# Kernel optimization log

Measured on AMD Instinct MI355X. Metric: run time of the kernel, lower is better.

The kernel has to match this reference:

```python
import jax, jax.numpy as jnp
import numpy as np

N_ATOMS = 8_000_000
N_REC = 2_000_000
N_POC = 500_000
N_CHAINS = 4


def setup_inputs() -> dict:
    key = jax.random.key(0)
    k1, k2, k3, k4 = jax.random.split(key, 4)
    # coordinates in nm, inside a ~5 nm box
    positions = jax.random.uniform(k1, (N_ATOMS, 3), dtype=jnp.float32) * 5.0
    box_vectors = jnp.diag(jnp.array([5.0, 5.0, 5.0], dtype=jnp.float32))
    # unique receptor atom indices into positions
    rec_indices = jax.random.permutation(k2, N_ATOMS)[:N_REC].astype(jnp.int32)
    # unique pocket indices INTO THE REC ARRAY (poc_pos = rec_pos[poc_indices])
    poc_indices = jax.random.permutation(k3, N_REC)[:N_POC].astype(jnp.int32)
    # contiguous chain assignment over rec atoms, all chains present in pocket
    chain_ids = ((jnp.arange(N_REC, dtype=jnp.int32) * N_CHAINS) // N_REC).astype(jnp.int32)
    poc_chain_ids = chain_ids[poc_indices]
    ref_poc = jax.random.uniform(k4, (N_POC, 3), dtype=jnp.float32) * 5.0
    k = jnp.float32(100.0)  # kJ/mol/nm^2
    return {
        "positions": positions, "box_vectors": box_vectors, "ref_poc": ref_poc,
        "k": k, "rec_indices": rec_indices, "poc_indices": poc_indices,
        "chain_ids": chain_ids, "poc_chain_ids": poc_chain_ids, "n_chains": N_CHAINS,
    }


def best_periodic_translation(pos1, pos2, box_vectors):
    # pos1, pos2: [C,3]; box_vectors: [3,3] (rows are lattice vectors)
    delta = pos2 - pos1
    inv = 1.0 / jnp.diag(box_vectors)
    s3 = jnp.round(delta[:, 2] * inv[2])
    delta = delta - s3[:, None] * box_vectors[2]
    s2 = jnp.round(delta[:, 1] * inv[1])
    delta = delta - s2[:, None] * box_vectors[1]
    s1 = jnp.round(delta[:, 0] * inv[0])
    return s1[:, None] * box_vectors[0] + s2[:, None] * box_vectors[1] + s3[:, None] * box_vectors[2]


def reference(positions, box_vectors, ref_poc, k, rec_indices, poc_indices, chain_ids, poc_chain_ids, n_chains):
    rec_pos = positions[rec_indices]  # [R,3]
    # Per-chain pocket COM. NOTE: original indexes global positions here
    # (positions[poc_chain_indices]), NOT rec_pos -- reproduced faithfully.
    poc_glob = positions[poc_indices]  # [P,3]
    counts = jax.ops.segment_sum(jnp.ones((poc_glob.shape[0],), poc_glob.dtype), poc_chain_ids, num_segments=n_chains)  # [C]
    poc_com = jax.ops.segment_sum(poc_glob, poc_chain_ids, num_segments=n_chains) / counts[:, None]  # [C,3]
    ref_com = jax.ops.segment_sum(ref_poc, poc_chain_ids, num_segments=n_chains) / counts[:, None]  # [C,3]
    best_t = best_periodic_translation(poc_com, ref_com, box_vectors)  # [C,3]
    rec_pos = rec_pos + best_t[chain_ids]  # translate each chain into the reference image

    poc_pos = rec_pos[poc_indices]  # [P,3]
    rec_origin = jnp.mean(rec_pos, axis=0)
    rec_centered = rec_pos - rec_origin
    r_sq = jnp.sum(rec_centered ** 2, axis=1)  # [R]
    F = jnp.zeros_like(rec_pos).at[poc_indices].set(-2.0 * k * (poc_pos - ref_poc))
    F_mean = jnp.mean(F, axis=0)
    torque = jnp.cross(rec_centered, F)
    torque_mean = jnp.mean(torque, axis=0)
    F_rot = jnp.cross(torque_mean[None], rec_centered) / r_sq[:, None]
    F_final = jnp.zeros_like(positions).at[rec_indices].set(F_mean + F_rot)
    return (jnp.float32(0.0), F_final)
```

## Files before the change

### kernel.cpp

```cpp
#include <hip/hip_runtime.h>


typedef unsigned int uint32;
typedef unsigned char uchar;

#define MAXC 16
#define W_BT 0
#define W_O 48
#define W_FM 52
#define W_TM 56
#define W_ACC 64

#define GCOUNT_OFF 4096
#define REC_OFF 8192
#define NB 512
#define BSH 14
#define BUCKET_ATOMS (1 << BSH)
#define CAP 5120
#define INV8_OFF (REC_OFF + NB * CAP * 4)

#define PB 512
#define RB 512
#define K1_KPT 16
#define K1_CHUNK (256 * K1_KPT)

struct PartSh { uint32 hist[NB]; uint32 curs[NB]; uint32 base[NB]; };
struct PocSh  { float red[4][43]; float accL[3 + MAXC * 10]; };
union ShU { PartSh part; PocSh poc; };

__device__ inline float waveSum(float v) {
#pragma unroll
  for (int off = 32; off > 0; off >>= 1) v += __shfl_down(v, off, 64);
  return v;
}

__global__ __launch_bounds__(256) void k_fused(
    const float* __restrict__ pos, const float* __restrict__ ref_poc,
    const int* __restrict__ rec_idx, const int* __restrict__ cid,
    const int* __restrict__ poc_idx, const int* __restrict__ poc_cid,
    const int* __restrict__ ncp, int R, int P,
    uint32* __restrict__ gcount, uint32* __restrict__ grecords,
    float* __restrict__ ws) {
  const int tid = threadIdx.x;
  const int bid = blockIdx.x;
  __shared__ ShU sh;
  const int C = ncp[0];

  if (bid < PB) {
    const int gsz = PB * 256;
    if (C <= 4) {
      float vals[43];
#pragma unroll
      for (int v = 0; v < 43; ++v) vals[v] = 0.f;
      for (int rb = bid * 256 + tid; rb < P; rb += 4 * gsz) {
        int rr[4], i2[4], c2[4], ri[4];
        float g[4][3], p[4][3], rf[4][3];
#pragma unroll
        for (int q = 0; q < 4; ++q) {
          int r = rb + q * gsz;
          rr[q] = (r < P) ? r : -1;
        }
#pragma unroll
        for (int q = 0; q < 4; ++q) {
          int r = (rr[q] < 0) ? 0 : rr[q];
          i2[q] = poc_idx[r];
          c2[q] = poc_cid[r];
        }
#pragma unroll
        for (int q = 0; q < 4; ++q) {
          ri[q] = rec_idx[i2[q]];
          g[q][0] = pos[3 * i2[q] + 0];
          g[q][1] = pos[3 * i2[q] + 1];
          g[q][2] = pos[3 * i2[q] + 2];
        }
#pragma unroll
        for (int q = 0; q < 4; ++q) {
          int r = (rr[q] < 0) ? 0 : rr[q];
          p[q][0] = pos[3 * ri[q] + 0];
          p[q][1] = pos[3 * ri[q] + 1];
          p[q][2] = pos[3 * ri[q] + 2];
          rf[q][0] = ref_poc[3 * r + 0];
          rf[q][1] = ref_poc[3 * r + 1];
          rf[q][2] = ref_poc[3 * r + 2];
        }
#pragma unroll
        for (int q = 0; q < 4; ++q) {
          if (rr[q] >= 0) {
            vals[0] += p[q][1] * rf[q][2] - p[q][2] * rf[q][1];
            vals[1] += p[q][2] * rf[q][0] - p[q][0] * rf[q][2];
            vals[2] += p[q][0] * rf[q][1] - p[q][1] * rf[q][0];
#pragma unroll
            for (int cc = 0; cc < 4; ++cc) {
              bool m = (c2[q] == cc);
              float* a = &vals[3 + cc * 10];
              a[0] += m ? g[q][0] : 0.f; a[1] += m ? g[q][1] : 0.f;
              a[2] += m ? g[q][2] : 0.f;
              a[3] += m ? rf[q][0] : 0.f; a[4] += m ? rf[q][1] : 0.f;
              a[5] += m ? rf[q][2] : 0.f;
              a[6] += m ? p[q][0] : 0.f; a[7] += m ? p[q][1] : 0.f;
              a[8] += m ? p[q][2] : 0.f;
              a[9] += m ? 1.f : 0.f;
            }
          }
        }
      }
      const int wid = tid >> 6;
#pragma unroll
      for (int v = 0; v < 43; ++v) {
        float s = waveSum(vals[v]);
        if ((tid & 63) == 0) sh.poc.red[wid][v] = s;
      }
      __syncthreads();
      for (int t = tid; t < 43; t += 256)
        atomicAdd(&ws[W_ACC + 19 + t], sh.poc.red[0][t] + sh.poc.red[1][t] +
                                       sh.poc.red[2][t] + sh.poc.red[3][t]);
    } else {
      float* accL = sh.poc.accL;
      for (int t = tid; t < 3 + MAXC * 10; t += 256) accL[t] = 0.f;
      __syncthreads();
      for (int r = bid * 256 + tid; r < P; r += PB * 256) {
        int i2 = poc_idx[r];
        int c2 = poc_cid[r];
        int ri = rec_idx[i2];
        float gx = pos[3 * i2 + 0], gy = pos[3 * i2 + 1], gz = pos[3 * i2 + 2];
        float px = pos[3 * ri + 0], py = pos[3 * ri + 1], pz = pos[3 * ri + 2];
        float rx = ref_poc[3 * r + 0], ry = ref_poc[3 * r + 1], rz = ref_poc[3 * r + 2];
        atomicAdd(&accL[0], py * rz - pz * ry);
        atomicAdd(&accL[1], pz * rx - px * rz);
        atomicAdd(&accL[2], px * ry - py * rx);
        float* a = &accL[3 + c2 * 10];
        atomicAdd(&a[0], gx); atomicAdd(&a[1], gy); atomicAdd(&a[2], gz);
        atomicAdd(&a[3], rx); atomicAdd(&a[4], ry); atomicAdd(&a[5], rz);
        atomicAdd(&a[6], px); atomicAdd(&a[7], py); atomicAdd(&a[8], pz);
        atomicAdd(&a[9], 1.f);
      }
      __syncthreads();
      for (int t = tid; t < 3 + MAXC * 10; t += 256)
        if (accL[t] != 0.f) atomicAdd(&ws[W_ACC + 19 + t], accL[t]);
    }
  } else {
    const int pb = bid - PB;
    uint32* hist = sh.part.hist;
    uint32* curs = sh.part.curs;
    uint32* base = sh.part.base;
    for (int r0 = pb * K1_CHUNK; r0 < R; r0 += RB * K1_CHUNK) {
      int cnt = R - r0; if (cnt > K1_CHUNK) cnt = K1_CHUNK;
      for (int t = tid; t < NB; t += 256) { hist[t] = 0u; curs[t] = 0u; }
      __syncthreads();
      uint32 enc[K1_KPT];
#pragma unroll
      for (int j = 0; j < K1_KPT; ++j) {
        int t = tid + j * 256;
        uint32 e = 0xFFFFFFFFu;
        if (t < cnt) {
          uint32 idx = (uint32)rec_idx[r0 + t];
          uint32 c = (uint32)cid[r0 + t] & 255u;
          e = (idx << 8) | c;
          atomicAdd(&hist[idx >> BSH], 1u);
        }
        enc[j] = e;
      }
      __syncthreads();
      for (int t = tid; t < NB; t += 256) {
        uint32 h = hist[t];
        base[t] = h ? atomicAdd(&gcount[t], h) : 0u;
      }
      __syncthreads();
#pragma unroll
      for (int j = 0; j < K1_KPT; ++j) {
        uint32 e = enc[j];
        if (e != 0xFFFFFFFFu) {
          uint32 b = e >> (8 + BSH);
          uint32 slot = base[b] + atomicAdd(&curs[b], 1u);
          if (slot < CAP) grecords[b * CAP + slot] = e;
        }
      }
      __syncthreads();
    }
  }
}

__global__ __launch_bounds__(256) void k_bucket_build(
    const float4* __restrict__ pos4, const int* __restrict__ ncp,
    const uint32* __restrict__ gcount, const uint32* __restrict__ grecords,
    int N, uchar* __restrict__ inv8, float* __restrict__ ws) {
  const int tid = threadIdx.x;
  const int b = blockIdx.x;
  const int a0 = b << BSH;
  if (a0 >= N) return;
  int natoms = N - a0; if (natoms > BUCKET_ATOMS) natoms = BUCKET_ATOMS;

  __shared__ uchar map_[BUCKET_ATOMS];
  __shared__ float cnt16[MAXC];
  uint4* m16 = (uint4*)map_;
  uint4 ff; ff.x = ff.y = ff.z = ff.w = 0xFFFFFFFFu;
  for (int t = tid; t < BUCKET_ATOMS / 16; t += 256) m16[t] = ff;
  const int C = ncp[0];
  if (C > 4) for (int t = tid; t < MAXC; t += 256) cnt16[t] = 0.f;
  __syncthreads();

  int n = (int)gcount[b]; if (n > CAP) n = CAP;
  float c0 = 0.f, c1 = 0.f, c2 = 0.f, c3 = 0.f;
  for (int t = tid; t < n; t += 256) {
    uint32 e = grecords[b * CAP + t];
    uint32 ia = (e >> 8) & (BUCKET_ATOMS - 1);
    uint32 c = e & 255u;
    map_[ia] = (uchar)c;
    if (C <= 4) {
      c0 += (c == 0u) ? 1.f : 0.f;
      c1 += (c == 1u) ? 1.f : 0.f;
      c2 += (c == 2u) ? 1.f : 0.f;
      c3 += (c == 3u) ? 1.f : 0.f;
    } else {
      atomicAdd(&cnt16[c], 1.f);
    }
  }
  __syncthreads();

  uchar* dst = inv8 + a0;
  if (natoms == BUCKET_ATOMS) {
    uint4* d16 = (uint4*)dst;
    for (int t = tid; t < BUCKET_ATOMS / 16; t += 256) d16[t] = m16[t];
  } else {
    for (int t = tid; t < natoms; t += 256) dst[t] = map_[t];
  }

  float sx = 0.f, sy = 0.f, sz = 0.f;
  int ngf = natoms >> 2;
  const uchar4* m4 = (const uchar4*)map_;
  int g0 = a0 >> 2;
  for (int g = tid; g < ngf; g += 256) {
    float4 p0 = pos4[3 * (g0 + g) + 0];
    float4 p1 = pos4[3 * (g0 + g) + 1];
    float4 p2 = pos4[3 * (g0 + g) + 2];
    uchar4 m = m4[g];
    if (m.x != 255) { sx += p0.x; sy += p0.y; sz += p0.z; }
    if (m.y != 255) { sx += p0.w; sy += p1.x; sz += p1.y; }
    if (m.z != 255) { sx += p1.z; sy += p1.w; sz += p2.x; }
    if (m.w != 255) { sx += p2.y; sy += p2.z; sz += p2.w; }
  }
  int tb = natoms & 3;
  if (tid < tb) {
    int a = a0 + (ngf << 2) + tid;
    const float* pf = (const float*)pos4;
    if (map_[(ngf << 2) + tid] != 255) {
      sx += pf[3 * a]; sy += pf[3 * a + 1]; sz += pf[3 * a + 2];
    }
  }

  __shared__ float red[4][7];
  float vv[7] = {sx, sy, sz, c0, c1, c2, c3};
  const int wid = tid >> 6;
#pragma unroll
  for (int v = 0; v < 7; ++v) {
    float s = waveSum(vv[v]);
    if ((tid & 63) == 0) red[wid][v] = s;
  }
  __syncthreads();
  if (tid < 7) {
    float s = red[0][tid] + red[1][tid] + red[2][tid] + red[3][tid];
    atomicAdd(&ws[W_ACC + tid], s);
  }
  if (C > 4 && tid < C) atomicAdd(&ws[W_ACC + 3 + tid], cnt16[tid]);
}

__global__ void k_finalize(const float* __restrict__ box,
                           const float* __restrict__ kp,
                           const int* __restrict__ ncp,
                           int R, float* __restrict__ ws) {
  __shared__ float tot[192];
  const int C = ncp[0];
  for (int t = threadIdx.x; t < 192; t += blockDim.x) tot[t] = ws[W_ACC + t];
  __syncthreads();
  if (threadIdx.x != 0) return;
  const float kk = kp[0];
  const float Rf = (float)R;
  const float* xp = &tot[19];
  float inv0 = 1.f / box[0], inv1 = 1.f / box[4], inv2 = 1.f / box[8];
  float ox = tot[0], oy = tot[1], oz = tot[2];
  float Fx = 0, Fy = 0, Fz = 0;
  float T1x = 0, T1y = 0, T1z = 0, T2x = 0, T2y = 0, T2z = 0;
  for (int c = 0; c < C; ++c) {
    float nrec = tot[3 + c];
    const float* a = &tot[22 + c * 10];
    float np = a[9];
    float invn = 1.f / np;
    float pcx = a[0] * invn, pcy = a[1] * invn, pcz = a[2] * invn;
    float rcx = a[3] * invn, rcy = a[4] * invn, rcz = a[5] * invn;
    float dx = rcx - pcx, dy = rcy - pcy, dz = rcz - pcz;
    float s3 = rintf(dz * inv2);
    dx -= s3 * box[6]; dy -= s3 * box[7]; dz -= s3 * box[8];
    float s2 = rintf(dy * inv1);
    dx -= s2 * box[3]; dy -= s2 * box[4]; dz -= s2 * box[5];
    float s1 = rintf(dx * inv0);
    float btx = s1 * box[0] + s2 * box[3] + s3 * box[6];
    float bty = s1 * box[1] + s2 * box[4] + s3 * box[7];
    float btz = s1 * box[2] + s2 * box[5] + s3 * box[8];
    ws[W_BT + c * 3 + 0] = btx;
    ws[W_BT + c * 3 + 1] = bty;
    ws[W_BT + c * 3 + 2] = btz;
    ox += nrec * btx; oy += nrec * bty; oz += nrec * btz;
    float SFx = -2.f * kk * (a[6] + np * btx - a[3]);
    float SFy = -2.f * kk * (a[7] + np * bty - a[4]);
    float SFz = -2.f * kk * (a[8] + np * btz - a[5]);
    Fx += SFx; Fy += SFy; Fz += SFz;
    T1x += a[7] * btz - a[8] * bty;
    T1y += a[8] * btx - a[6] * btz;
    T1z += a[6] * bty - a[7] * btx;
    T2x += bty * SFz - btz * SFy;
    T2y += btz * SFx - btx * SFz;
    T2z += btx * SFy - bty * SFx;
  }
  ox /= Rf; oy /= Rf; oz /= Rf;
  float Tx = 2.f * kk * xp[0] - 2.f * kk * T1x + T2x - (oy * Fz - oz * Fy);
  float Ty = 2.f * kk * xp[1] - 2.f * kk * T1y + T2y - (oz * Fx - ox * Fz);
  float Tz = 2.f * kk * xp[2] - 2.f * kk * T1z + T2z - (ox * Fy - oy * Fx);
  ws[W_O + 0] = ox; ws[W_O + 1] = oy; ws[W_O + 2] = oz;
  ws[W_FM + 0] = Fx / Rf; ws[W_FM + 1] = Fy / Rf; ws[W_FM + 2] = Fz / Rf;
  ws[W_TM + 0] = Tx / Rf; ws[W_TM + 1] = Ty / Rf; ws[W_TM + 2] = Tz / Rf;
}

__global__ __launch_bounds__(256) void k_final_dense(
    const float* __restrict__ pos, const uchar* __restrict__ inv8,
    int N, const float* __restrict__ ws, float* __restrict__ out) {
  __shared__ float stage[3328];
  __shared__ float sc[64];
  const int tid = threadIdx.x;
  if (tid < 64) sc[tid] = ws[tid];
  const int t0 = blockIdx.x * 1024;
  int nat = N - t0; if (nat > 1024) nat = 1024;
  const int nfl = nat * 3;

  if (nat == 1024) {
    const float4* src4 = (const float4*)(pos + 3 * t0);
#pragma unroll
    for (int kk = 0; kk < 3; ++kk) {
      int v4 = tid + kk * 256;
      float4 p = src4[v4];
      int idx = 4 * v4 + v4 / 3;
      stage[idx + 0] = p.x; stage[idx + 1] = p.y;
      stage[idx + 2] = p.z; stage[idx + 3] = p.w;
    }
  } else {
    for (int k = tid; k < nfl; k += 256)
      stage[k + (int)((unsigned)k / 12u)] = pos[3 * t0 + k];
  }
  __syncthreads();

  float ox = sc[W_O + 0], oy = sc[W_O + 1], oz = sc[W_O + 2];
  float fmx = sc[W_FM + 0], fmy = sc[W_FM + 1], fmz = sc[W_FM + 2];
  float tmx = sc[W_TM + 0], tmy = sc[W_TM + 1], tmz = sc[W_TM + 2];

  uchar mc[4];
  if (nat == 1024) {
    uchar4 m = ((const uchar4*)(inv8 + t0))[tid];
    mc[0] = m.x; mc[1] = m.y; mc[2] = m.z; mc[3] = m.w;
  } else {
#pragma unroll
    for (int q = 0; q < 4; ++q) {
      int la = 4 * tid + q;
      mc[q] = (la < nat) ? inv8[t0 + la] : (uchar)255;
    }
  }
#pragma unroll
  for (int q = 0; q < 4; ++q) {
    int la = 4 * tid + q;
    if (la < nat) {
      float* s = &stage[13 * tid + 3 * q];
      float fx = 0.f, fy = 0.f, fz = 0.f;
      int c = mc[q];
      if (c != 255) {
        float cx = s[0] + sc[W_BT + 3 * c + 0] - ox;
        float cy = s[1] + sc[W_BT + 3 * c + 1] - oy;
        float cz = s[2] + sc[W_BT + 3 * c + 2] - oz;
        float inv = 1.f / (cx * cx + cy * cy + cz * cz);
        fx = fmx + (tmy * cz - tmz * cy) * inv;
        fy = fmy + (tmz * cx - tmx * cz) * inv;
        fz = fmz + (tmx * cy - tmy * cx) * inv;
      }
      s[0] = fx; s[1] = fy; s[2] = fz;
    }
  }
  __syncthreads();

  if (blockIdx.x == 0 && tid == 0) out[0] = 0.f;
  float* ob = out + 1 + 3 * t0;
  if (nat == 1024) {
#pragma unroll
    for (int kk = 0; kk < 3; ++kk) {
      int j = tid + kk * 256;
      if (j < 767) {
        int k = 3 + 4 * j;
        float4 v;
        v.x = stage[k + k / 12];
        v.y = stage[(k + 1) + (k + 1) / 12];
        v.z = stage[(k + 2) + (k + 2) / 12];
        v.w = stage[(k + 3) + (k + 3) / 12];
        *(float4*)(ob + k) = v;
      }
    }
    if (tid < 3) ob[tid] = stage[tid];
    if (tid == 3) ob[3071] = stage[3071 + 3071 / 12];
  } else {
    for (int k = tid; k < nfl; k += 256)
      ob[k] = stage[k + (int)((unsigned)k / 12u)];
  }
}

extern "C" void kernel_launch(void* const* d_in, const int* in_sizes, int n_in,
                              void* d_out, int out_size, void* d_ws, size_t ws_size,
                              hipStream_t stream) {
  const float* pos     = (const float*)d_in[0];
  const float* box     = (const float*)d_in[1];
  const float* ref_poc = (const float*)d_in[2];
  const float* kp      = (const float*)d_in[3];
  const int* rec_idx   = (const int*)d_in[4];
  const int* poc_idx   = (const int*)d_in[5];
  const int* cid       = (const int*)d_in[6];
  const int* poc_cid   = (const int*)d_in[7];
  const int* ncp       = (const int*)d_in[8];
  float* out = (float*)d_out;
  float* ws  = (float*)d_ws;
  uint32* gcount   = (uint32*)((char*)d_ws + GCOUNT_OFF);
  uint32* grecords = (uint32*)((char*)d_ws + REC_OFF);
  uchar* inv8      = (uchar*)d_ws + INV8_OFF;

  const int N = in_sizes[0] / 3;
  const int R = in_sizes[4];
  const int P = in_sizes[5];

  hipMemsetAsync(d_ws, 0, 8192, stream);

  k_fused<<<PB + RB, 256, 0, stream>>>(pos, ref_poc, rec_idx, cid, poc_idx,
                                       poc_cid, ncp, R, P, gcount, grecords, ws);
  k_bucket_build<<<NB, 256, 0, stream>>>((const float4*)pos, ncp, gcount,
                                         grecords, N, inv8, ws);
  k_finalize<<<1, 256, 0, stream>>>(box, kp, ncp, R, ws);
  int gF = (N + 1023) / 1024;
  k_final_dense<<<gF, 256, 0, stream>>>(pos, inv8, N, ws, out);
}
```

Before: 267.4 us.

## Replace bucketed partition with direct byte-map scatter and grid-stride position sum

Removes the two-phase bucket partition (global histogram, records buffer, per-bucket shared-memory map build). The inverse chain map is now filled by a memset to 0xFF, then written with direct scattered byte stores from rec_idx/cid, fused into the pocket-reduction kernel. A new grid-stride kernel then streams positions and the map to compute the receptor position sum and the per-chain counts. This drops the 40MB intermediate records traffic and the shared-memory staging, at the cost of random byte-granular global writes and an extra memset of N bytes.

```diff
diff --git a/kernel.cpp b/kernel.cpp
--- a/kernel.cpp
+++ b/kernel.cpp
@@ -11,22 +11,9 @@
 #define W_TM 56
 #define W_ACC 64
 
-#define GCOUNT_OFF 4096
-#define REC_OFF 8192
-#define NB 512
-#define BSH 14
-#define BUCKET_ATOMS (1 << BSH)
-#define CAP 5120
-#define INV8_OFF (REC_OFF + NB * CAP * 4)
-
-#define PB 512
-#define RB 512
-#define K1_KPT 16
-#define K1_CHUNK (256 * K1_KPT)
-
-struct PartSh { uint32 hist[NB]; uint32 curs[NB]; uint32 base[NB]; };
-struct PocSh  { float red[4][43]; float accL[3 + MAXC * 10]; };
-union ShU { PartSh part; PocSh poc; };
+#define INV8_OFF 8192
+#define K1B 1024
+#define PSB 2048
 
 __device__ inline float waveSum(float v) {
 #pragma unroll
@@ -39,216 +26,170 @@
     const int* __restrict__ rec_idx, const int* __restrict__ cid,
     const int* __restrict__ poc_idx, const int* __restrict__ poc_cid,
     const int* __restrict__ ncp, int R, int P,
-    uint32* __restrict__ gcount, uint32* __restrict__ grecords,
-    float* __restrict__ ws) {
+    uchar* __restrict__ inv8, float* __restrict__ ws) {
   const int tid = threadIdx.x;
   const int bid = blockIdx.x;
-  __shared__ ShU sh;
   const int C = ncp[0];
-
-  if (bid < PB) {
-    const int gsz = PB * 256;
-    if (C <= 4) {
-      float vals[43];
-#pragma unroll
-      for (int v = 0; v < 43; ++v) vals[v] = 0.f;
-      for (int rb = bid * 256 + tid; rb < P; rb += 4 * gsz) {
-        int rr[4], i2[4], c2[4], ri[4];
-        float g[4][3], p[4][3], rf[4][3];
-#pragma unroll
-        for (int q = 0; q < 4; ++q) {
-          int r = rb + q * gsz;
-          rr[q] = (r < P) ? r : -1;
-        }
-#pragma unroll
-        for (int q = 0; q < 4; ++q) {
-          int r = (rr[q] < 0) ? 0 : rr[q];
-          i2[q] = poc_idx[r];
-          c2[q] = poc_cid[r];
-        }
-#pragma unroll
-        for (int q = 0; q < 4; ++q) {
-          ri[q] = rec_idx[i2[q]];
-          g[q][0] = pos[3 * i2[q] + 0];
-          g[q][1] = pos[3 * i2[q] + 1];
-          g[q][2] = pos[3 * i2[q] + 2];
-        }
-#pragma unroll
-        for (int q = 0; q < 4; ++q) {
-          int r = (rr[q] < 0) ? 0 : rr[q];
-          p[q][0] = pos[3 * ri[q] + 0];
-          p[q][1] = pos[3 * ri[q] + 1];
-          p[q][2] = pos[3 * ri[q] + 2];
-          rf[q][0] = ref_poc[3 * r + 0];
-          rf[q][1] = ref_poc[3 * r + 1];
-          rf[q][2] = ref_poc[3 * r + 2];
-        }
-#pragma unroll
-        for (int q = 0; q < 4; ++q) {
-          if (rr[q] >= 0) {
-            vals[0] += p[q][1] * rf[q][2] - p[q][2] * rf[q][1];
-            vals[1] += p[q][2] * rf[q][0] - p[q][0] * rf[q][2];
-            vals[2] += p[q][0] * rf[q][1] - p[q][1] * rf[q][0];
-#pragma unroll
-            for (int cc = 0; cc < 4; ++cc) {
-              bool m = (c2[q] == cc);
-              float* a = &vals[3 + cc * 10];
-              a[0] += m ? g[q][0] : 0.f; a[1] += m ? g[q][1] : 0.f;
-              a[2] += m ? g[q][2] : 0.f;
-              a[3] += m ? rf[q][0] : 0.f; a[4] += m ? rf[q][1] : 0.f;
-              a[5] += m ? rf[q][2] : 0.f;
-              a[6] += m ? p[q][0] : 0.f; a[7] += m ? p[q][1] : 0.f;
-              a[8] += m ? p[q][2] : 0.f;
-              a[9] += m ? 1.f : 0.f;
-            }
+  __shared__ float red[4][43];
+  __shared__ float accL[3 + MAXC * 10];
+
+  const int gsz = K1B * 256;
+  if (C <= 4) {
+    float vals[43];
+#pragma unroll
+    for (int v = 0; v < 43; ++v) vals[v] = 0.f;
+    for (int rb = bid * 256 + tid; rb < P; rb += 4 * gsz) {
+      int rr[4], i2[4], c2[4], ri[4];
+      float g[4][3], p[4][3], rf[4][3];
+#pragma unroll
+      for (int q = 0; q < 4; ++q) {
+        int r = rb + q * gsz;
+        rr[q] = (r < P) ? r : -1;
+      }
+#pragma unroll
+      for (int q = 0; q < 4; ++q) {
+        int r = (rr[q] < 0) ? 0 : rr[q];
+        i2[q] = poc_idx[r];
+        c2[q] = poc_cid[r];
+      }
+#pragma unroll
+      for (int q = 0; q < 4; ++q) {
+        ri[q] = rec_idx[i2[q]];
+        g[q][0] = pos[3 * i2[q] + 0];
+        g[q][1] = pos[3 * i2[q] + 1];
+        g[q][2] = pos[3 * i2[q] + 2];
+      }
+#pragma unroll
+      for (int q = 0; q < 4; ++q) {
+        int r = (rr[q] < 0) ? 0 : rr[q];
+        p[q][0] = pos[3 * ri[q] + 0];
+        p[q][1] = pos[3 * ri[q] + 1];
+        p[q][2] = pos[3 * ri[q] + 2];
+        rf[q][0] = ref_poc[3 * r + 0];
+        rf[q][1] = ref_poc[3 * r + 1];
+        rf[q][2] = ref_poc[3 * r + 2];
+      }
+#pragma unroll
+      for (int q = 0; q < 4; ++q) {
+        if (rr[q] >= 0) {
+          vals[0] += p[q][1] * rf[q][2] - p[q][2] * rf[q][1];
+          vals[1] += p[q][2] * rf[q][0] - p[q][0] * rf[q][2];
+          vals[2] += p[q][0] * rf[q][1] - p[q][1] * rf[q][0];
+#pragma unroll
+          for (int cc = 0; cc < 4; ++cc) {
+            bool m = (c2[q] == cc);
+            float* a = &vals[3 + cc * 10];
+            a[0] += m ? g[q][0] : 0.f; a[1] += m ? g[q][1] : 0.f;
+            a[2] += m ? g[q][2] : 0.f;
+            a[3] += m ? rf[q][0] : 0.f; a[4] += m ? rf[q][1] : 0.f;
+            a[5] += m ? rf[q][2] : 0.f;
+            a[6] += m ? p[q][0] : 0.f; a[7] += m ? p[q][1] : 0.f;
+            a[8] += m ? p[q][2] : 0.f;
+            a[9] += m ? 1.f : 0.f;
           }
         }
       }
-      const int wid = tid >> 6;
-#pragma unroll
-      for (int v = 0; v < 43; ++v) {
-        float s = waveSum(vals[v]);
-        if ((tid & 63) == 0) sh.poc.red[wid][v] = s;
-      }
-      __syncthreads();
-      for (int t = tid; t < 43; t += 256)
-        atomicAdd(&ws[W_ACC + 19 + t], sh.poc.red[0][t] + sh.poc.red[1][t] +
-                                       sh.poc.red[2][t] + sh.poc.red[3][t]);
-    } else {
-      float* accL = sh.poc.accL;
-      for (int t = tid; t < 3 + MAXC * 10; t += 256) accL[t] = 0.f;
-      __syncthreads();
-      for (int r = bid * 256 + tid; r < P; r += PB * 256) {
-        int i2 = poc_idx[r];
-        int c2 = poc_cid[r];
-        int ri = rec_idx[i2];
-        float gx = pos[3 * i2 + 0], gy = pos[3 * i2 + 1], gz = pos[3 * i2 + 2];
-        float px = pos[3 * ri + 0], py = pos[3 * ri + 1], pz = pos[3 * ri + 2];
-        float rx = ref_poc[3 * r + 0], ry = ref_poc[3 * r + 1], rz = ref_poc[3 * r + 2];
-        atomicAdd(&accL[0], py * rz - pz * ry);
-        atomicAdd(&accL[1], pz * rx - px * rz);
-        atomicAdd(&accL[2], px * ry - py * rx);
-        float* a = &accL[3 + c2 * 10];
-        atomicAdd(&a[0], gx); atomicAdd(&a[1], gy); atomicAdd(&a[2], gz);
-        atomicAdd(&a[3], rx); atomicAdd(&a[4], ry); atomicAdd(&a[5], rz);
-        atomicAdd(&a[6], px); atomicAdd(&a[7], py); atomicAdd(&a[8], pz);
-        atomicAdd(&a[9], 1.f);
-      }
-      __syncthreads();
-      for (int t = tid; t < 3 + MAXC * 10; t += 256)
-        if (accL[t] != 0.f) atomicAdd(&ws[W_ACC + 19 + t], accL[t]);
-    }
+    }
+    const int wid = tid >> 6;
+#pragma unroll
+    for (int v = 0; v < 43; ++v) {
+      float s = waveSum(vals[v]);
+      if ((tid & 63) == 0) red[wid][v] = s;
+    }
+    __syncthreads();
+    for (int t = tid; t < 43; t += 256)
+      atomicAdd(&ws[W_ACC + 19 + t],
+                red[0][t] + red[1][t] + red[2][t] + red[3][t]);
   } else {
-    const int pb = bid - PB;
-    uint32* hist = sh.part.hist;
-    uint32* curs = sh.part.curs;
-    uint32* base = sh.part.base;
-    for (int r0 = pb * K1_CHUNK; r0 < R; r0 += RB * K1_CHUNK) {
-      int cnt = R - r0; if (cnt > K1_CHUNK) cnt = K1_CHUNK;
-      for (int t = tid; t < NB; t += 256) { hist[t] = 0u; curs[t] = 0u; }
-      __syncthreads();
-      uint32 enc[K1_KPT];
-#pragma unroll
-      for (int j = 0; j < K1_KPT; ++j) {
-        int t = tid + j * 256;
-        uint32 e = 0xFFFFFFFFu;
-        if (t < cnt) {
-          uint32 idx = (uint32)rec_idx[r0 + t];
-          uint32 c = (uint32)cid[r0 + t] & 255u;
-          e = (idx << 8) | c;
-          atomicAdd(&hist[idx >> BSH], 1u);
-        }
-        enc[j] = e;
-      }
-      __syncthreads();
-      for (int t = tid; t < NB; t += 256) {
-        uint32 h = hist[t];
-        base[t] = h ? atomicAdd(&gcount[t], h) : 0u;
-      }
-      __syncthreads();
-#pragma unroll
-      for (int j = 0; j < K1_KPT; ++j) {
-        uint32 e = enc[j];
-        if (e != 0xFFFFFFFFu) {
-          uint32 b = e >> (8 + BSH);
-          uint32 slot = base[b] + atomicAdd(&curs[b], 1u);
-          if (slot < CAP) grecords[b * CAP + slot] = e;
-        }
-      }
-      __syncthreads();
-    }
-  }
-}
-
-__global__ __launch_bounds__(256) void k_bucket_build(
-    const float4* __restrict__ pos4, const int* __restrict__ ncp,
-    const uint32* __restrict__ gcount, const uint32* __restrict__ grecords,
-    int N, uchar* __restrict__ inv8, float* __restrict__ ws) {
+    for (int t = tid; t < 3 + MAXC * 10; t += 256) accL[t] = 0.f;
+    __syncthreads();
+    for (int r = bid * 256 + tid; r < P; r += K1B * 256) {
+      int i2 = poc_idx[r];
+      int c2 = poc_cid[r];
+      int ri = rec_idx[i2];
+      float gx = pos[3 * i2 + 0], gy = pos[3 * i2 + 1], gz = pos[3 * i2 + 2];
+      float px = pos[3 * ri + 0], py = pos[3 * ri + 1], pz = pos[3 * ri + 2];
+      float rx = ref_poc[3 * r + 0], ry = ref_poc[3 * r + 1], rz = ref_poc[3 * r + 2];
+      atomicAdd(&accL[0], py * rz - pz * ry);
+      atomicAdd(&accL[1], pz * rx - px * rz);
+      atomicAdd(&accL[2], px * ry - py * rx);
+      float* a = &accL[3 + c2 * 10];
+      atomicAdd(&a[0], gx); atomicAdd(&a[1], gy); atomicAdd(&a[2], gz);
+      atomicAdd(&a[3], rx); atomicAdd(&a[4], ry); atomicAdd(&a[5], rz);
+      atomicAdd(&a[6], px); atomicAdd(&a[7], py); atomicAdd(&a[8], pz);
+      atomicAdd(&a[9], 1.f);
+    }
+    __syncthreads();
+    for (int t = tid; t < 3 + MAXC * 10; t += 256)
+      if (accL[t] != 0.f) atomicAdd(&ws[W_ACC + 19 + t], accL[t]);
+  }
+
+  const int nv = R >> 2;
+  for (int t = bid * 256 + tid; t < nv; t += K1B * 256) {
+    int4 i4 = ((const int4*)rec_idx)[t];
+    int4 c4 = ((const int4*)cid)[t];
+    inv8[i4.x] = (uchar)c4.x;
+    inv8[i4.y] = (uchar)c4.y;
+    inv8[i4.z] = (uchar)c4.z;
+    inv8[i4.w] = (uchar)c4.w;
+  }
+  for (int t = (nv << 2) + bid * 256 + tid; t < R; t += K1B * 256)
+    inv8[rec_idx[t]] = (uchar)cid[t];
+}
+
+__global__ __launch_bounds__(256) void k_possum(
+    const float4* __restrict__ pos4, const uchar* __restrict__ inv8,
+    const int* __restrict__ ncp, int N, float* __restrict__ ws) {
   const int tid = threadIdx.x;
-  const int b = blockIdx.x;
-  const int a0 = b << BSH;
-  if (a0 >= N) return;
-  int natoms = N - a0; if (natoms > BUCKET_ATOMS) natoms = BUCKET_ATOMS;
-
-  __shared__ uchar map_[BUCKET_ATOMS];
+  const int C = ncp[0];
+  __shared__ float red[4][7];
   __shared__ float cnt16[MAXC];
-  uint4* m16 = (uint4*)map_;
-  uint4 ff; ff.x = ff.y = ff.z = ff.w = 0xFFFFFFFFu;
-  for (int t = tid; t < BUCKET_ATOMS / 16; t += 256) m16[t] = ff;
-  const int C = ncp[0];
-  if (C > 4) for (int t = tid; t < MAXC; t += 256) cnt16[t] = 0.f;
-  __syncthreads();
-
-  int n = (int)gcount[b]; if (n > CAP) n = CAP;
+  if (C > 4) {
+    for (int t = tid; t < MAXC; t += 256) cnt16[t] = 0.f;
+    __syncthreads();
+  }
+  float sx = 0.f, sy = 0.f, sz = 0.f;
   float c0 = 0.f, c1 = 0.f, c2 = 0.f, c3 = 0.f;
-  for (int t = tid; t < n; t += 256) {
-    uint32 e = grecords[b * CAP + t];
-    uint32 ia = (e >> 8) & (BUCKET_ATOMS - 1);
-    uint32 c = e & 255u;
-    map_[ia] = (uchar)c;
-    if (C <= 4) {
-      c0 += (c == 0u) ? 1.f : 0.f;
-      c1 += (c == 1u) ? 1.f : 0.f;
-      c2 += (c == 2u) ? 1.f : 0.f;
-      c3 += (c == 3u) ? 1.f : 0.f;
-    } else {
-      atomicAdd(&cnt16[c], 1.f);
-    }
-  }
-  __syncthreads();
-
-  uchar* dst = inv8 + a0;
-  if (natoms == BUCKET_ATOMS) {
-    uint4* d16 = (uint4*)dst;
-    for (int t = tid; t < BUCKET_ATOMS / 16; t += 256) d16[t] = m16[t];
-  } else {
-    for (int t = tid; t < natoms; t += 256) dst[t] = map_[t];
-  }
-
-  float sx = 0.f, sy = 0.f, sz = 0.f;
-  int ngf = natoms >> 2;
-  const uchar4* m4 = (const uchar4*)map_;
-  int g0 = a0 >> 2;
-  for (int g = tid; g < ngf; g += 256) {
-    float4 p0 = pos4[3 * (g0 + g) + 0];
-    float4 p1 = pos4[3 * (g0 + g) + 1];
-    float4 p2 = pos4[3 * (g0 + g) + 2];
+  const int ng = N >> 2;
+  const uchar4* m4 = (const uchar4*)inv8;
+  for (int g = blockIdx.x * 256 + tid; g < ng; g += PSB * 256) {
+    float4 p0 = pos4[3 * g + 0];
+    float4 p1 = pos4[3 * g + 1];
+    float4 p2 = pos4[3 * g + 2];
     uchar4 m = m4[g];
     if (m.x != 255) { sx += p0.x; sy += p0.y; sz += p0.z; }
     if (m.y != 255) { sx += p0.w; sy += p1.x; sz += p1.y; }
     if (m.z != 255) { sx += p1.z; sy += p1.w; sz += p2.x; }
     if (m.w != 255) { sx += p2.y; sy += p2.z; sz += p2.w; }
-  }
-  int tb = natoms & 3;
-  if (tid < tb) {
-    int a = a0 + (ngf << 2) + tid;
-    const float* pf = (const float*)pos4;
-    if (map_[(ngf << 2) + tid] != 255) {
+    if (C <= 4) {
+      c0 += ((m.x == 0) ? 1.f : 0.f) + ((m.y == 0) ? 1.f : 0.f) +
+            ((m.z == 0) ? 1.f : 0.f) + ((m.w == 0) ? 1.f : 0.f);
+      c1 += ((m.x == 1) ? 1.f : 0.f) + ((m.y == 1) ? 1.f : 0.f) +
+            ((m.z == 1) ? 1.f : 0.f) + ((m.w == 1) ? 1.f : 0.f);
+      c2 += ((m.x == 2) ? 1.f : 0.f) + ((m.y == 2) ? 1.f : 0.f) +
+            ((m.z == 2) ? 1.f : 0.f) + ((m.w == 2) ? 1.f : 0.f);
+      c3 += ((m.x == 3) ? 1.f : 0.f) + ((m.y == 3) ? 1.f : 0.f) +
+            ((m.z == 3) ? 1.f : 0.f) + ((m.w == 3) ? 1.f : 0.f);
+    } else {
+      if (m.x != 255) atomicAdd(&cnt16[m.x], 1.f);
+      if (m.y != 255) atomicAdd(&cnt16[m.y], 1.f);
+      if (m.z != 255) atomicAdd(&cnt16[m.z], 1.f);
+      if (m.w != 255) atomicAdd(&cnt16[m.w], 1.f);
+    }
+  }
+  const float* pf = (const float*)pos4;
+  for (int a = (ng << 2) + blockIdx.x * 256 + tid; a < N; a += PSB * 256) {
+    uchar m = inv8[a];
+    if (m != 255) {
       sx += pf[3 * a]; sy += pf[3 * a + 1]; sz += pf[3 * a + 2];
-    }
-  }
-
-  __shared__ float red[4][7];
+      if (C <= 4) {
+        c0 += (m == 0) ? 1.f : 0.f; c1 += (m == 1) ? 1.f : 0.f;
+        c2 += (m == 2) ? 1.f : 0.f; c3 += (m == 3) ? 1.f : 0.f;
+      } else {
+        atomicAdd(&cnt16[m], 1.f);
+      }
+    }
+  }
   float vv[7] = {sx, sy, sz, c0, c1, c2, c3};
   const int wid = tid >> 6;
 #pragma unroll
@@ -421,20 +362,18 @@
   const int* ncp       = (const int*)d_in[8];
   float* out = (float*)d_out;
   float* ws  = (float*)d_ws;
-  uint32* gcount   = (uint32*)((char*)d_ws + GCOUNT_OFF);
-  uint32* grecords = (uint32*)((char*)d_ws + REC_OFF);
-  uchar* inv8      = (uchar*)d_ws + INV8_OFF;
+  uchar* inv8 = (uchar*)d_ws + INV8_OFF;
 
   const int N = in_sizes[0] / 3;
   const int R = in_sizes[4];
   const int P = in_sizes[5];
 
   hipMemsetAsync(d_ws, 0, 8192, stream);
-
-  k_fused<<<PB + RB, 256, 0, stream>>>(pos, ref_poc, rec_idx, cid, poc_idx,
-                                       poc_cid, ncp, R, P, gcount, grecords, ws);
-  k_bucket_build<<<NB, 256, 0, stream>>>((const float4*)pos, ncp, gcount,
-                                         grecords, N, inv8, ws);
+  hipMemsetAsync((char*)d_ws + INV8_OFF, 0xFF, (size_t)N, stream);
+
+  k_fused<<<K1B, 256, 0, stream>>>(pos, ref_poc, rec_idx, cid, poc_idx,
+                                   poc_cid, ncp, R, P, inv8, ws);
+  k_possum<<<PSB, 256, 0, stream>>>((const float4*)pos, inv8, ncp, N, ws);
   k_finalize<<<1, 256, 0, stream>>>(box, kp, ncp, R, ws);
   int gF = (N + 1023) / 1024;
   k_final_dense<<<gF, 256, 0, stream>>>(pos, inv8, N, ws, out);
```

After: 304.3 us. 13.8% more time.
